# Optimization experiments

Hardware: AMD Instinct MI355X
Metric: run time of the kernel (lower is better)

Reference implementation:

```python
import jax, jax.numpy as jnp
import numpy as np

B, L, D, H = 2, 4096, 768, 12
HS = D // H  # head_size = 64
SCALE = HS ** -0.5


def setup_inputs() -> dict:
    key = jax.random.key(0)
    k1, k2, k3 = jax.random.split(key, 3)
    x = jax.random.normal(k1, (B, L, D), dtype=jnp.float32)
    # torch nn.Linear weights are [out_features, in_features]; y = x @ W.T
    Wq = jax.random.normal(k2, (D, D), dtype=jnp.float32) * (D ** -0.5)
    Wo = jax.random.normal(k3, (D, D), dtype=jnp.float32) * (D ** -0.5)
    return {"x": x, "Wq": Wq, "Wo": Wo}


def reference(x, Wq, Wo):
    b, l, d = x.shape
    # NOTE: source module uses self.query for Q, K, AND V (bug preserved).
    q = jnp.einsum('bld,ed->ble', x, Wq)              # [B,L,D]
    q = q.reshape(b, l, H, HS).transpose(0, 2, 1, 3)   # [B,H,L,HS]
    k = v = q                                          # K = V = Q (faithful)
    scores = jnp.einsum('bhqd,bhkd->bhqk', q, k) * SCALE  # [B,H,L,L]
    attn = jax.nn.softmax(scores, axis=-1)
    out = jnp.einsum('bhqk,bhkd->bhqd', attn, v)       # [B,H,L,HS]
    out = out.transpose(0, 2, 1, 3).reshape(b, l, d)   # [B,L,D]
    out = jnp.einsum('bld,ed->ble', out, Wo)           # output projection
    return out
```

## Files before the change

kernel.cpp:

```cpp
#include <hip/hip_runtime.h>
#include <hip/hip_bf16.h>

#define LQ 4096
#define DQ 768
#define NH 12
#define NB 2

typedef __attribute__((ext_vector_type(8))) short short8;
typedef __attribute__((ext_vector_type(2))) unsigned uint2v;
typedef __attribute__((ext_vector_type(4))) float f32x4;

__device__ __forceinline__ short f2bf(float f) {
    union { float f; unsigned u; } v; v.f = f;
    unsigned r = v.u + 0x7FFFu + ((v.u >> 16) & 1u);
    return (short)(r >> 16);
}

__device__ __forceinline__ unsigned pk2(float a, float b) {
    float2 t; t.x = a; t.y = b;
    __hip_bfloat162 h = __float22bfloat162_rn(t);
    unsigned u; __builtin_memcpy(&u, &h, 4);
    return u;
}

__device__ __forceinline__ f32x4 mfma16(short8 a, short8 b, f32x4 c) {
    return __builtin_amdgcn_mfma_f32_16x16x32_bf16(a, b, c, 0, 0, 0);
}

#define SQRT_C 0.424660891f

__global__ __launch_bounds__(256) void cvtw(const float* __restrict__ a,
                                            short* __restrict__ o) {
    int i = blockIdx.x * 256 + threadIdx.x;
    float4 v = ((const float4*)a)[i];
    *(uint2v*)&o[i * 4] = (uint2v){pk2(v.x, v.y), pk2(v.z, v.w)};
}


template <int MODE>
__global__ __launch_bounds__(256, 3) void gemm_nt(const short* __restrict__ A,
                                                  const float* __restrict__ W,
                                                  void* __restrict__ Cp,
                                                  short* __restrict__ Vf) {
    __shared__ short As[128 * 72];
    __shared__ short Bs[64 * 72];
    const int t = threadIdx.x;
    const int lane = t & 63, w = t >> 6;
    const int lr = lane & 15, qd = lane >> 4;
    const int wm = (w & 1) * 64, wn = (w >> 1) * 32;
    const int lin = blockIdx.x;
    const int xcd = lin & 7, jj = lin >> 3;
    const int nt = jj % 12, mt = (jj / 12) * 8 + xcd;
    const int m0 = mt * 128, n0 = nt * 64;

    f32x4 acc[4][2];
#pragma unroll
    for (int i = 0; i < 4; ++i)
#pragma unroll
        for (int j = 0; j < 2; ++j) acc[i][j] = (f32x4){0.f, 0.f, 0.f, 0.f};

#pragma unroll
    for (int u = 0; u < 4; ++u) {
        int c = t + 256 * u, row = c >> 3, col = (c & 7) << 3;
        *(short8*)&As[row * 72 + col] = *(const short8*)&A[(size_t)(m0 + row) * DQ + col];
    }
#pragma unroll
    for (int u = 0; u < 4; ++u) {
        int c = t + 256 * u, row = c >> 4, col = (c & 15) << 2;
        float4 v = *(const float4*)&W[(size_t)(n0 + row) * DQ + col];
        *(uint2v*)&Bs[row * 72 + col] = (uint2v){pk2(v.x, v.y), pk2(v.z, v.w)};
    }
    __syncthreads();

    for (int kt = 0; kt < 12; ++kt) {
        short8 ra[4]; float4 rb[4];
        if (kt < 11) {
            const int k0 = (kt + 1) * 64;
#pragma unroll
            for (int u = 0; u < 4; ++u) {
                int c = t + 256 * u, row = c >> 3, col = (c & 7) << 3;
                ra[u] = *(const short8*)&A[(size_t)(m0 + row) * DQ + k0 + col];
            }
#pragma unroll
            for (int u = 0; u < 4; ++u) {
                int c = t + 256 * u, row = c >> 4, col = (c & 15) << 2;
                rb[u] = *(const float4*)&W[(size_t)(n0 + row) * DQ + k0 + col];
            }
        }
#pragma unroll
        for (int s = 0; s < 2; ++s) {
            short8 af[4], bf[2];
#pragma unroll
            for (int i = 0; i < 4; ++i)
                af[i] = *(short8*)&As[(wm + 16 * i + lr) * 72 + 32 * s + qd * 8];
#pragma unroll
            for (int j = 0; j < 2; ++j)
                bf[j] = *(short8*)&Bs[(wn + 16 * j + lr) * 72 + 32 * s + qd * 8];
#pragma unroll
            for (int i = 0; i < 4; ++i)
#pragma unroll
                for (int j = 0; j < 2; ++j)
                    acc[i][j] = mfma16(af[i], bf[j], acc[i][j]);
        }
        if (kt < 11) {
            __syncthreads();
#pragma unroll
            for (int u = 0; u < 4; ++u) {
                int c = t + 256 * u, row = c >> 3, col = (c & 7) << 3;
                *(short8*)&As[row * 72 + col] = ra[u];
            }
#pragma unroll
            for (int u = 0; u < 4; ++u) {
                int c = t + 256 * u, row = c >> 4, col = (c & 15) << 2;
                *(uint2v*)&Bs[row * 72 + col] = (uint2v){pk2(rb[u].x, rb[u].y), pk2(rb[u].z, rb[u].w)};
            }
            __syncthreads();
        }
    }

    if (MODE == 0) {
#pragma unroll
        for (int i = 0; i < 4; ++i)
#pragma unroll
            for (int j = 0; j < 2; ++j) {
                const int row0 = m0 + wm + 16 * i + qd * 4;
                const int col = n0 + wn + 16 * j + lr;
#pragma unroll
                for (int r = 0; r < 4; ++r)
                    ((float*)Cp)[(size_t)(row0 + r) * DQ + col] = acc[i][j][r];
            }
    } else {
        short* Qf = (short*)Cp;
        short* F = As;
        const int bh = (m0 >> 12) * NH + nt;
        const size_t gbase = (size_t)bh * (LQ * 64) + (size_t)(((m0 & 4095) >> 6) << 12);
        __syncthreads();
#pragma unroll
        for (int i = 0; i < 4; ++i)
#pragma unroll
            for (int j = 0; j < 2; ++j) {
                const int kl = wm + 16 * i + qd * 4;
                const int hs = wn + 16 * j + lr;
                const int fi = ((kl >> 6) << 12) + ((((hs >> 4) << 1) + ((kl >> 5) & 1)) << 9)
                             + (((hs & 15) + (((kl >> 3) & 3) << 4)) << 3) + (kl & 7);
                *(uint2v*)&F[fi] = (uint2v){pk2(acc[i][j][0], acc[i][j][1]),
                                            pk2(acc[i][j][2], acc[i][j][3])};
            }
        __syncthreads();
#pragma unroll
        for (int p = 0; p < 4; ++p) {
            int u = t + 256 * p;
            *(short8*)&Vf[gbase + (size_t)u * 8] = *(short8*)&F[u * 8];
        }
        __syncthreads();
#pragma unroll
        for (int i = 0; i < 4; ++i)
#pragma unroll
            for (int j = 0; j < 2; ++j) {
                const int hs = wn + 16 * j + lr;
#pragma unroll
                for (int r = 0; r < 4; ++r) {
                    const int key = wm + 16 * i + qd * 4 + r;
                    const int fi = ((key >> 6) << 12) + (((((key >> 4) & 3) << 1) + (hs >> 5)) << 9)
                                 + (((qd * 4 + r) + (((hs >> 3) & 3) << 4)) << 3) + (hs & 7);
                    F[fi] = f2bf(acc[i][j][r] * SQRT_C);
                }
            }
        __syncthreads();
#pragma unroll
        for (int p = 0; p < 4; ++p) {
            int u = t + 256 * p;
            *(short8*)&Qf[gbase + (size_t)u * 8] = *(short8*)&F[u * 8];
        }
    }
}

__global__ __launch_bounds__(128, 2) void attn(const short* __restrict__ Qf,
                                               const short* __restrict__ Vf,
                                               short* __restrict__ O) {
    const int linear = blockIdx.x;
    const int xcd = linear & 7, slot = linear >> 3;
    const int bh = 3 * xcd + (slot >> 5);
    const int qtile = slot & 31;
    const int t = threadIdx.x;
    const int lane = t & 63, w = t >> 6;
    const int lr = lane & 15, qd = lane >> 4;

    __shared__ short Ps[2][4][16 * 72];

    const short* Qbh = Qf + (size_t)bh * (LQ * 64);
    const short* Vbh = Vf + (size_t)bh * (LQ * 64);
    const int q0 = qtile * 128 + w * 64;

    const short one_bf = (short)0x3F80;
    short8 ones;
#pragma unroll
    for (int j = 0; j < 8; ++j) ones[j] = one_bf;

    short8 aq[4][2];
#pragma unroll
    for (int i = 0; i < 4; ++i) {
        const int g = (q0 >> 4) + i;
#pragma unroll
        for (int s = 0; s < 2; ++s)
            aq[i][s] = *(const short8*)&Qbh[g * 1024 + s * 512 + lane * 8];
    }

    f32x4 oacc[4][4], lacc[4];
#pragma unroll
    for (int i = 0; i < 4; ++i) {
        lacc[i] = (f32x4){0.f, 0.f, 0.f, 0.f};
#pragma unroll
        for (int t2 = 0; t2 < 4; ++t2) oacc[i][t2] = (f32x4){0.f, 0.f, 0.f, 0.f};
    }

    short8 kf[4][2];
#pragma unroll
    for (int t4 = 0; t4 < 4; ++t4)
#pragma unroll
        for (int s = 0; s < 2; ++s)
            kf[t4][s] = *(const short8*)&Qbh[(t4 * 2 + s) * 512 + lane * 8];

    for (int kb = 0; kb < LQ / 64; ++kb) {
        short8 vb[4][2];
#pragma unroll
        for (int t2 = 0; t2 < 4; ++t2)
#pragma unroll
            for (int ks = 0; ks < 2; ++ks)
                vb[t2][ks] = *(const short8*)&Vbh[kb * 4096 + (t2 * 2 + ks) * 512 + lane * 8];
        short8 kfn[4][2];
        if (kb < LQ / 64 - 1) {
#pragma unroll
            for (int t4 = 0; t4 < 4; ++t4)
#pragma unroll
                for (int s = 0; s < 2; ++s)
                    kfn[t4][s] = *(const short8*)&Qbh[(kb + 1) * 4096 + (t4 * 2 + s) * 512 + lane * 8];
        }

#pragma unroll
        for (int i = 0; i < 4; ++i) {
            f32x4 sacc[4];
#pragma unroll
            for (int t4 = 0; t4 < 4; ++t4) {
                sacc[t4] = (f32x4){0.f, 0.f, 0.f, 0.f};
#pragma unroll
                for (int s = 0; s < 2; ++s)
                    sacc[t4] = mfma16(kf[t4][s], aq[i][s], sacc[t4]);
            }
#pragma unroll
            for (int t4 = 0; t4 < 4; ++t4) {
                float p0 = __builtin_amdgcn_exp2f(sacc[t4][0]);
                float p1 = __builtin_amdgcn_exp2f(sacc[t4][1]);
                float p2 = __builtin_amdgcn_exp2f(sacc[t4][2]);
                float p3 = __builtin_amdgcn_exp2f(sacc[t4][3]);
                *(uint2v*)&Ps[w][i][lr * 72 + 16 * t4 + 4 * qd] =
                    (uint2v){pk2(p0, p1), pk2(p2, p3)};
            }
#pragma unroll
            for (int ks = 0; ks < 2; ++ks) {
                short8 pa = *(short8*)&Ps[w][i][lr * 72 + 32 * ks + qd * 8];
#pragma unroll
                for (int t2 = 0; t2 < 4; ++t2)
                    oacc[i][t2] = mfma16(pa, vb[t2][ks], oacc[i][t2]);
                lacc[i] = mfma16(pa, ones, lacc[i]);
            }
        }
#pragma unroll
        for (int t4 = 0; t4 < 4; ++t4)
#pragma unroll
            for (int s = 0; s < 2; ++s) kf[t4][s] = kfn[t4][s];
    }

    const int b = bh / NH, h = bh % NH;
#pragma unroll
    for (int i = 0; i < 4; ++i) {
        float inv[4];
#pragma unroll
        for (int r = 0; r < 4; ++r) inv[r] = 1.0f / lacc[i][r];
#pragma unroll
        for (int t2 = 0; t2 < 4; ++t2)
#pragma unroll
            for (int r = 0; r < 4; ++r) {
                int lq = q0 + 16 * i + qd * 4 + r;
                int e = h * 64 + 16 * t2 + lr;
                O[((size_t)(b * LQ + lq)) * DQ + e] = f2bf(oacc[i][t2][r] * inv[r]);
            }
    }
}

extern "C" void kernel_launch(void* const* d_in, const int* in_sizes, int n_in,
                              void* d_out, int out_size, void* d_ws, size_t ws_size,
                              hipStream_t stream) {
    (void)in_sizes; (void)n_in; (void)out_size; (void)ws_size;
    const float* x  = (const float*)d_in[0];
    const float* Wq = (const float*)d_in[1];
    const float* Wo = (const float*)d_in[2];
    float* out = (float*)d_out;

    const size_t NQ = (size_t)NB * NH * LQ * 64;
    short* Qf  = (short*)d_ws;
    short* Vfb = Qf + NQ;
    short* Ows = Vfb + NQ;

    cvtw<<<(NB * LQ * DQ) / 1024, 256, 0, stream>>>(x, Ows);
    gemm_nt<1><<<768, 256, 0, stream>>>(Ows, Wq, Qf, Vfb);
    attn<<<768, 128, 0, stream>>>(Qf, Vfb, Ows);
    gemm_nt<0><<<768, 256, 0, stream>>>(Ows, Wo, out, nullptr);
}
```

Before: 252.8 us.

## Split attention key range across two wave pairs and merge partials via LDS

Each attention block now has four waves instead of two. Each pair of waves processes half of the key blocks for the same 128 queries, and the second half's output and row-sum accumulators are added into the first half through shared memory before normalization. This doubles the number of waves per block and halves each wave's serial loop, aiming to give more latency hiding and better occupancy. The cost is a larger shared-memory footprint, extra synchronization and a reduction step. Register pressure under the new launch bounds could limit occupancy.

```diff
diff --git a/kernel.cpp b/kernel.cpp
--- a/kernel.cpp
+++ b/kernel.cpp
@@ -175,7 +175,7 @@
     }
 }
 
-__global__ __launch_bounds__(128, 2) void attn(const short* __restrict__ Qf,
+__global__ __launch_bounds__(256, 3) void attn(const short* __restrict__ Qf,
                                                const short* __restrict__ Vf,
                                                short* __restrict__ O) {
     const int linear = blockIdx.x;
@@ -184,13 +184,16 @@
     const int qtile = slot & 31;
     const int t = threadIdx.x;
     const int lane = t & 63, w = t >> 6;
+    const int qw = w & 1, half = w >> 1;
     const int lr = lane & 15, qd = lane >> 4;
 
-    __shared__ short Ps[2][4][16 * 72];
+    __shared__ alignas(16) char smem[43008];
+    short* Ps = (short*)smem + w * (4 * 16 * 72);
 
     const short* Qbh = Qf + (size_t)bh * (LQ * 64);
     const short* Vbh = Vf + (size_t)bh * (LQ * 64);
-    const int q0 = qtile * 128 + w * 64;
+    const int q0 = qtile * 128 + qw * 64;
+    const int kb0 = half * (LQ / 128);
 
     const short one_bf = (short)0x3F80;
     short8 ones;
@@ -219,9 +222,9 @@
     for (int t4 = 0; t4 < 4; ++t4)
 #pragma unroll
         for (int s = 0; s < 2; ++s)
-            kf[t4][s] = *(const short8*)&Qbh[(t4 * 2 + s) * 512 + lane * 8];
-
-    for (int kb = 0; kb < LQ / 64; ++kb) {
+            kf[t4][s] = *(const short8*)&Qbh[kb0 * 4096 + (t4 * 2 + s) * 512 + lane * 8];
+
+    for (int kb = kb0; kb < kb0 + LQ / 128; ++kb) {
         short8 vb[4][2];
 #pragma unroll
         for (int t2 = 0; t2 < 4; ++t2)
@@ -229,7 +232,7 @@
             for (int ks = 0; ks < 2; ++ks)
                 vb[t2][ks] = *(const short8*)&Vbh[kb * 4096 + (t2 * 2 + ks) * 512 + lane * 8];
         short8 kfn[4][2];
-        if (kb < LQ / 64 - 1) {
+        if (kb < kb0 + LQ / 128 - 1) {
 #pragma unroll
             for (int t4 = 0; t4 < 4; ++t4)
 #pragma unroll
@@ -253,12 +256,12 @@
                 float p1 = __builtin_amdgcn_exp2f(sacc[t4][1]);
                 float p2 = __builtin_amdgcn_exp2f(sacc[t4][2]);
                 float p3 = __builtin_amdgcn_exp2f(sacc[t4][3]);
-                *(uint2v*)&Ps[w][i][lr * 72 + 16 * t4 + 4 * qd] =
+                *(uint2v*)&Ps[i * (16 * 72) + lr * 72 + 16 * t4 + 4 * qd] =
                     (uint2v){pk2(p0, p1), pk2(p2, p3)};
             }
 #pragma unroll
             for (int ks = 0; ks < 2; ++ks) {
-                short8 pa = *(short8*)&Ps[w][i][lr * 72 + 32 * ks + qd * 8];
+                short8 pa = *(short8*)&Ps[i * (16 * 72) + lr * 72 + 32 * ks + qd * 8];
 #pragma unroll
                 for (int t2 = 0; t2 < 4; ++t2)
                     oacc[i][t2] = mfma16(pa, vb[t2][ks], oacc[i][t2]);
@@ -269,6 +272,26 @@
         for (int t4 = 0; t4 < 4; ++t4)
 #pragma unroll
             for (int s = 0; s < 2; ++s) kf[t4][s] = kfn[t4][s];
+    }
+
+    __syncthreads();
+    f32x4* ex = (f32x4*)smem + (qw * 64 + lane) * 21;
+    if (half) {
+#pragma unroll
+        for (int i = 0; i < 4; ++i) {
+#pragma unroll
+            for (int t2 = 0; t2 < 4; ++t2) ex[i * 4 + t2] = oacc[i][t2];
+            ex[16 + i] = lacc[i];
+        }
+    }
+    __syncthreads();
+    if (half) return;
+
+#pragma unroll
+    for (int i = 0; i < 4; ++i) {
+#pragma unroll
+        for (int t2 = 0; t2 < 4; ++t2) oacc[i][t2] += ex[i * 4 + t2];
+        lacc[i] += ex[16 + i];
     }
 
     const int b = bh / NH, h = bh % NH;
@@ -304,6 +327,6 @@
 
     cvtw<<<(NB * LQ * DQ) / 1024, 256, 0, stream>>>(x, Ows);
     gemm_nt<1><<<768, 256, 0, stream>>>(Ows, Wq, Qf, Vfb);
-    attn<<<768, 128, 0, stream>>>(Qf, Vfb, Ows);
+    attn<<<768, 256, 0, stream>>>(Qf, Vfb, Ows);
     gemm_nt<0><<<768, 256, 0, stream>>>(Ows, Wo, out, nullptr);
 }
```

New measurement: 557.7 us. 121% more time.
